# Performance work log

Measured on AMD Instinct MI355X. Metric: run time of the kernel, lower is better.

The kernel has to match this reference:

```python
import jax, jax.numpy as jnp
import numpy as np

G, N = 1024, 40            # graphs, nodes per graph (complete graphs)
SLOPE = 0.1                # leaky relu negative slope
SMAT_IDX = jnp.array([0, 1, 2, 3, 1, 4, 5, 6, 2, 5, 7, 8, 3, 6, 8, 9])


def setup_inputs() -> dict:
    key = jax.random.key(0)
    ks = jax.random.split(key, 24)

    # --- graph structure: G identical complete graphs of N nodes ---
    ii, jj = np.meshgrid(np.arange(N), np.arange(N), indexing="ij")
    mask = ii != jj
    src_l, dst_l = ii[mask], jj[mask]              # directed edges per graph
    offs = (np.arange(G) * N)[:, None]
    edge_index = np.stack([(src_l[None] + offs).ravel(),
                           (dst_l[None] + offs).ravel()]).astype(np.int64)
    iu, ju = np.triu_indices(N, 1)
    M = iu.shape[0]                                 # 780 undirected edges
    ud_edges = np.stack([iu, ju], 1).astype(np.int64)
    edge_map = np.zeros((N, N), np.int64)
    edge_map[iu, ju] = np.arange(M)
    edge_map[ju, iu] = np.arange(M)

    def w(k, shape, fan_in):
        return jax.random.normal(k, shape, jnp.float32) / np.sqrt(fan_in)

    inp = {
        "x": jax.random.normal(ks[0], (G * N, 16), jnp.float32),
        "edge_index": jnp.asarray(edge_index),
        "ud_edges": jnp.asarray(ud_edges),
        "edge_map": jnp.asarray(edge_map),
        # GCN stack 6->32->32->64
        "Wg0": w(ks[1], (6, 32), 6),   "bg0": jnp.zeros((32,), jnp.float32),
        "Wg1": w(ks[2], (32, 32), 32), "bg1": jnp.zeros((32,), jnp.float32),
        "Wg2": w(ks[3], (32, 64), 32), "bg2": jnp.zeros((64,), jnp.float32),
        # node MLP 64->64->64->10
        "Wn0": w(ks[4], (64, 64), 64), "bn0": jnp.zeros((64,), jnp.float32),
        "Wn1": w(ks[5], (64, 64), 64), "bn1": jnp.zeros((64,), jnp.float32),
        "Wn2": w(ks[6], (64, 10), 64), "bn2": jnp.zeros((10,), jnp.float32),
        # edge MLP 64->64->64->10
        "We0": w(ks[7], (64, 64), 64), "be0": jnp.zeros((64,), jnp.float32),
        "We1": w(ks[8], (64, 64), 64), "be1": jnp.zeros((64,), jnp.float32),
        "We2": w(ks[9], (64, 10), 64), "be2": jnp.zeros((10,), jnp.float32),
    }
    return inp


def _forward(x, edge_index, ud_edges, edge_map,
             Wg0, bg0, Wg1, bg1, Wg2, bg2,
             Wn0, bn0, Wn1, bn1, Wn2, bn2,
             We0, be0, We1, be1, We2, be2):
    num_nodes = x.shape[0]
    h = x[:, :6]                                   # node_feature_mode == 1
    src, dst = edge_index[0], edge_index[1]

    # GCN normalization (add_self_loops=False, edge_weight=1)
    deg = jax.ops.segment_sum(jnp.ones(src.shape[0], x.dtype), dst,
                              num_segments=num_nodes)
    dis = jnp.where(deg > 0, jax.lax.rsqrt(jnp.maximum(deg, 1e-12)), 0.0)
    norm = dis[src] * dis[dst]                     # [E]

    def gcn(h, W, b):
        m = (h @ W)[src] * norm[:, None]
        return jax.ops.segment_sum(m, dst, num_segments=num_nodes) + b

    # eval mode: dropout is identity
    h = jax.nn.leaky_relu(gcn(h, Wg0, bg0), SLOPE)
    h = jax.nn.leaky_relu(gcn(h, Wg1, bg1), SLOPE)
    h = gcn(h, Wg2, bg2)                           # [G*N, 64]

    hg = h.reshape(G, N, -1)                       # [G, N, 64]

    def mlp(z, Ws, bs):
        for W, b in zip(Ws[:-1], bs[:-1]):
            z = jax.nn.leaky_relu(z @ W + b, SLOPE)
        return z @ Ws[-1] + bs[-1]

    vp = mlp(hg, [Wn0, Wn1, Wn2], [bn0, bn1, bn2])            # [G, N, 10]
    e = hg[:, ud_edges[:, 0], :] + hg[:, ud_edges[:, 1], :]   # [G, M, 64]
    ep = mlp(e, [We0, We1, We2], [be0, be1, be2])             # [G, M, 10]

    # recover_X: diag blocks smat(vp[i]), off-diag smat(ep[edge_map[i,j]])
    epm = ep[:, edge_map, :]                                  # [G, N, N, 10]
    eye = jnp.eye(N, dtype=bool)[None, :, :, None]
    vecs = jnp.where(eye, vp[:, :, None, :], epm)             # [G, N, N, 10]
    blocks = vecs[..., SMAT_IDX].reshape(G, N, N, 4, 4)
    X = blocks.transpose(0, 1, 3, 2, 4).reshape(G, 4 * N, 4 * N)
    return h, X


def reference(x, edge_index, ud_edges, edge_map,
              Wg0, bg0, Wg1, bg1, Wg2, bg2,
              Wn0, bn0, Wn1, bn1, Wn2, bn2,
              We0, be0, We1, be1, We2, be2):
    return _forward(x, edge_index, ud_edges, edge_map,
                    Wg0, bg0, Wg1, bg1, Wg2, bg2,
                    Wn0, bn0, Wn1, bn1, Wn2, bn2,
                    We0, be0, We1, be1, We2, be2)
```

## Files before the change

### kernel.cpp

```cpp
#include <hip/hip_runtime.h>

#define G_GRAPHS 1024
#define N_NODES  40
#define M_EDGES  780
#define NUM_NODES (G_GRAPHS * N_NODES)
#define H_ELEMS  (NUM_NODES * 64)
#define X_STRIDE 160
#define X_PER_G  25600
#define SLOPE 0.1f

#define EDGE_BLOCKS 6240
#define VP_BLOCKS   320
#define PACK_PER_MLP 9216

typedef __bf16 bf16x8 __attribute__((ext_vector_type(8)));
typedef unsigned short us8 __attribute__((ext_vector_type(8)));
typedef float f32x4 __attribute__((ext_vector_type(4)));

__device__ __forceinline__ float lrelu(float v) { return fmaxf(v, SLOPE * v); }
__device__ __forceinline__ unsigned short f2bf(float x) {
    __bf16 b = (__bf16)x;
    return __builtin_bit_cast(unsigned short, b);
}
__device__ __forceinline__ unsigned int pk2bf(float a, float b) {
    return (unsigned int)f2bf(a) | ((unsigned int)f2bf(b) << 16);
}

__global__ __launch_bounds__(256) void k_prep(const float* __restrict__ We0,
                                              const float* __restrict__ We1,
                                              const float* __restrict__ We2,
                                              const float* __restrict__ Wn0,
                                              const float* __restrict__ Wn1,
                                              const float* __restrict__ Wn2,
                                              unsigned short* __restrict__ wp) {
    int t = blockIdx.x * 256 + threadIdx.x;
    int mlp = t / PACK_PER_MLP;
    int o = t - mlp * PACK_PER_MLP;
    const float* W0 = mlp ? Wn0 : We0;
    const float* W1 = mlp ? Wn1 : We1;
    const float* W2 = mlp ? Wn2 : We2;
    float val;
    if (o < 8192) {
        const float* W = (o < 4096) ? W0 : W1;
        int idx = o & 4095;
        int j = idx & 7, l = (idx >> 3) & 63, tt = idx >> 9;
        int kt = tt & 1, mt = tt >> 1;
        int k = kt * 32 + ((l >> 4) & 3) * 8 + j;
        int m = mt * 16 + (l & 15);
        val = W[k * 64 + m];
    } else {
        int idx = o - 8192;
        int j = idx & 7, l = (idx >> 3) & 63, kt = idx >> 9;
        int k = kt * 32 + ((l >> 4) & 3) * 8 + j;
        int m = l & 15;
        val = (m < 10) ? W2[k * 10 + m] : 0.f;
    }
    wp[mlp * PACK_PER_MLP + o] = f2bf(val);
}

__global__ __launch_bounds__(256) void k_gcn(const float* __restrict__ x,
                                             const float* __restrict__ Wg0,
                                             const float* __restrict__ bg0,
                                             const float* __restrict__ Wg1,
                                             const float* __restrict__ bg1,
                                             const float* __restrict__ Wg2,
                                             const float* __restrict__ bg2,
                                             float* __restrict__ hout) {
    __shared__ float h0[N_NODES * 6];
    __shared__ float buf[N_NODES * 64];
    __shared__ float S[64];
    __shared__ float P[8 * 64];
    __shared__ float h1[N_NODES * 32];
    __shared__ float h2[N_NODES * 32];

    const int g = blockIdx.x;
    const int tid = threadIdx.x;
    const float inv39 = 1.0f / 39.0f;

    for (int idx = tid; idx < N_NODES * 6; idx += 256) {
        int n = idx / 6, f = idx - n * 6;
        h0[idx] = x[(g * N_NODES + n) * 16 + f];
    }
    __syncthreads();

    for (int idx = tid; idx < N_NODES * 32; idx += 256) {
        int n = idx >> 5, c = idx & 31;
        float s = 0.f;
#pragma unroll
        for (int f = 0; f < 6; f++) s += h0[n * 6 + f] * Wg0[f * 32 + c];
        buf[n * 32 + c] = s;
    }
    __syncthreads();
    { int c = tid & 31, grp = tid >> 5; float s = 0.f;
#pragma unroll
      for (int n = grp * 5; n < grp * 5 + 5; n++) s += buf[n * 32 + c];
      P[grp * 32 + c] = s; }
    __syncthreads();
    if (tid < 32) { float s = 0.f;
#pragma unroll
      for (int grp = 0; grp < 8; grp++) s += P[grp * 32 + tid];
      S[tid] = s; }
    __syncthreads();
    for (int idx = tid; idx < N_NODES * 32; idx += 256) {
        int n = idx >> 5, c = idx & 31;
        h1[idx] = lrelu((S[c] - buf[n * 32 + c]) * inv39 + bg0[c]);
    }
    __syncthreads();

    for (int idx = tid; idx < N_NODES * 32; idx += 256) {
        int n = idx >> 5, c = idx & 31;
        float s = 0.f;
#pragma unroll
        for (int m = 0; m < 32; m++) s += h1[n * 32 + m] * Wg1[m * 32 + c];
        buf[n * 32 + c] = s;
    }
    __syncthreads();
    { int c = tid & 31, grp = tid >> 5; float s = 0.f;
#pragma unroll
      for (int n = grp * 5; n < grp * 5 + 5; n++) s += buf[n * 32 + c];
      P[grp * 32 + c] = s; }
    __syncthreads();
    if (tid < 32) { float s = 0.f;
#pragma unroll
      for (int grp = 0; grp < 8; grp++) s += P[grp * 32 + tid];
      S[tid] = s; }
    __syncthreads();
    for (int idx = tid; idx < N_NODES * 32; idx += 256) {
        int n = idx >> 5, c = idx & 31;
        h2[idx] = lrelu((S[c] - buf[n * 32 + c]) * inv39 + bg1[c]);
    }
    __syncthreads();

    for (int idx = tid; idx < N_NODES * 64; idx += 256) {
        int n = idx >> 6, c = idx & 63;
        float s = 0.f;
#pragma unroll
        for (int m = 0; m < 32; m++) s += h2[n * 32 + m] * Wg2[m * 64 + c];
        buf[idx] = s;
    }
    __syncthreads();
    { int c = tid & 63, grp = tid >> 6; float s = 0.f;
#pragma unroll
      for (int n = grp * 10; n < grp * 10 + 10; n++) s += buf[n * 64 + c];
      P[grp * 64 + c] = s; }
    __syncthreads();
    if (tid < 64) { float s = 0.f;
#pragma unroll
      for (int grp = 0; grp < 4; grp++) s += P[grp * 64 + tid];
      S[tid] = s; }
    __syncthreads();
    for (int idx = tid; idx < N_NODES * 64; idx += 256) {
        int n = idx >> 6, c = idx & 63;
        hout[(g * N_NODES + n) * 64 + c] = (S[c] - buf[n * 64 + c]) * inv39 + bg2[c];
    }
}

__global__ __launch_bounds__(256) void k_mlp(const float* __restrict__ h,
                                             const unsigned short* __restrict__ wp,
                                             const float* __restrict__ be0,
                                             const float* __restrict__ be1,
                                             const float* __restrict__ be2,
                                             const float* __restrict__ bn0,
                                             const float* __restrict__ bn1,
                                             const float* __restrict__ bn2,
                                             float* __restrict__ X) {
    __shared__ __align__(16) unsigned short sE[128 * 64];
    __shared__ __align__(16) unsigned short sZ[128 * 64];

    const int tid = threadIdx.x;
    const int l = tid & 63;
    const int w = tid >> 6;
    const int bid = blockIdx.x;
    const bool is_edge = (bid < EDGE_BLOCKS);

    const unsigned short* wb = wp + (is_edge ? 0 : PACK_PER_MLP);
    const float* b0 = is_edge ? be0 : bn0;
    const float* b1 = is_edge ? be1 : bn1;
    const float* b2 = is_edge ? be2 : bn2;

    const int r = 32 * w + (l >> 1);
    const int hf = l & 1;
    int g, i = 0, j = 0;
    if (is_edge) {
        int eid = bid * 128 + r;
        g = eid / M_EDGES;
        int m = eid - g * M_EDGES;
        int rem = m;
        while (rem >= (N_NODES - 1) - i) { rem -= (N_NODES - 1) - i; ++i; }
        j = i + 1 + rem;
    } else {
        int nid = (bid - EDGE_BLOCKS) * 128 + r;
        g = nid / N_NODES;
        i = nid - g * N_NODES;
        j = i;
    }

    {
        const float4* pa = (const float4*)(h + (g * N_NODES + i) * 64 + hf * 32);
        const float4* pb = (const float4*)(h + (g * N_NODES + j) * 64 + hf * 32);
        unsigned short tmp[32];
#pragma unroll
        for (int q = 0; q < 8; q++) {
            float4 a = pa[q];
            if (is_edge) {
                float4 b = pb[q];
                a.x += b.x; a.y += b.y; a.z += b.z; a.w += b.w;
            }
            tmp[4 * q + 0] = f2bf(a.x); tmp[4 * q + 1] = f2bf(a.y);
            tmp[4 * q + 2] = f2bf(a.z); tmp[4 * q + 3] = f2bf(a.w);
        }
#pragma unroll
        for (int q = 0; q < 4; q++) {
            int cs = (hf * 4 + q) ^ (r & 7);
            *(us8*)((char*)sE + r * 128 + cs * 16) = *(const us8*)(tmp + 8 * q);
        }
    }

    const int nl = l & 15;
    const int rq = (l >> 4) & 3;

    auto WA = [&](const unsigned short* base, int mt, int kt) -> bf16x8 {
        return __builtin_bit_cast(bf16x8,
            *(const us8*)(base + ((mt * 2 + kt) * 64 + l) * 8));
    };
    auto ZB = [&](const unsigned short* s, int nt, int kt) -> bf16x8 {
        int node = 32 * w + nt * 16 + nl;
        int cs = (kt * 4 + rq) ^ (node & 7);
        return __builtin_bit_cast(bf16x8,
            *(const us8*)((const char*)s + node * 128 + cs * 16));
    };
    auto zstore = [&](unsigned short* s, int mt, int nt, const f32x4& v) {
        int node = 32 * w + nt * 16 + nl;
        int cs = (mt * 2 + (rq >> 1)) ^ (node & 7);
        uint2 u = make_uint2(pk2bf(v[0], v[1]), pk2bf(v[2], v[3]));
        *(uint2*)((char*)s + node * 128 + cs * 16 + (rq & 1) * 8) = u;
    };

    {
        bf16x8 B[2][2];
#pragma unroll
        for (int nt = 0; nt < 2; nt++)
#pragma unroll
            for (int kt = 0; kt < 2; kt++) B[nt][kt] = ZB(sE, nt, kt);
#pragma unroll
        for (int mt = 0; mt < 4; mt++) {
            bf16x8 A0 = WA(wb, mt, 0), A1 = WA(wb, mt, 1);
            float4 bv = *(const float4*)(b0 + mt * 16 + rq * 4);
#pragma unroll
            for (int nt = 0; nt < 2; nt++) {
                f32x4 acc = (f32x4){0.f, 0.f, 0.f, 0.f};
                acc = __builtin_amdgcn_mfma_f32_16x16x32_bf16(A0, B[nt][0], acc, 0, 0, 0);
                acc = __builtin_amdgcn_mfma_f32_16x16x32_bf16(A1, B[nt][1], acc, 0, 0, 0);
                f32x4 z;
                z[0] = lrelu(acc[0] + bv.x); z[1] = lrelu(acc[1] + bv.y);
                z[2] = lrelu(acc[2] + bv.z); z[3] = lrelu(acc[3] + bv.w);
                zstore(sZ, mt, nt, z);
            }
        }
    }

    {
        bf16x8 B[2][2];
#pragma unroll
        for (int nt = 0; nt < 2; nt++)
#pragma unroll
            for (int kt = 0; kt < 2; kt++) B[nt][kt] = ZB(sZ, nt, kt);
        const unsigned short* w1p = wb + 4096;
#pragma unroll
        for (int mt = 0; mt < 4; mt++) {
            bf16x8 A0 = WA(w1p, mt, 0), A1 = WA(w1p, mt, 1);
            float4 bv = *(const float4*)(b1 + mt * 16 + rq * 4);
#pragma unroll
            for (int nt = 0; nt < 2; nt++) {
                f32x4 acc = (f32x4){0.f, 0.f, 0.f, 0.f};
                acc = __builtin_amdgcn_mfma_f32_16x16x32_bf16(A0, B[nt][0], acc, 0, 0, 0);
                acc = __builtin_amdgcn_mfma_f32_16x16x32_bf16(A1, B[nt][1], acc, 0, 0, 0);
                f32x4 z;
                z[0] = lrelu(acc[0] + bv.x); z[1] = lrelu(acc[1] + bv.y);
                z[2] = lrelu(acc[2] + bv.z); z[3] = lrelu(acc[3] + bv.w);
                zstore(sE, mt, nt, z);
            }
        }
    }

    float* sEPf = (float*)sZ + w * 1024;
    {
        bf16x8 B[2][2];
#pragma unroll
        for (int nt = 0; nt < 2; nt++)
#pragma unroll
            for (int kt = 0; kt < 2; kt++) B[nt][kt] = ZB(sE, nt, kt);
        const unsigned short* w2p = wb + 8192;
        bf16x8 A0 = WA(w2p, 0, 0), A1 = WA(w2p, 0, 1);
        float bz[4];
#pragma unroll
        for (int k = 0; k < 4; k++) {
            int f = rq * 4 + k;
            bz[k] = (f < 10) ? b2[f] : 0.f;
        }
#pragma unroll
        for (int nt = 0; nt < 2; nt++) {
            f32x4 acc = (f32x4){0.f, 0.f, 0.f, 0.f};
            acc = __builtin_amdgcn_mfma_f32_16x16x32_bf16(A0, B[nt][0], acc, 0, 0, 0);
            acc = __builtin_amdgcn_mfma_f32_16x16x32_bf16(A1, B[nt][1], acc, 0, 0, 0);
            int nl2 = nt * 16 + nl;
            float4 v = make_float4(acc[0] + bz[0], acc[1] + bz[1],
                                   acc[2] + bz[2], acc[3] + bz[3]);
            *(float4*)(sEPf + nl2 * 20 + rq * 4) = v;
        }
    }

    {
        const float* ep = sEPf + (r & 31) * 20;
        float4 e0 = *(const float4*)(ep + 0);
        float4 e1 = *(const float4*)(ep + 4);
        float4 e2 = *(const float4*)(ep + 8);
        float4 r0 = make_float4(e0.x, e0.y, e0.z, e0.w);
        float4 r1 = make_float4(e0.y, e1.x, e1.y, e1.z);
        float4 r2 = make_float4(e0.z, e1.y, e1.w, e2.x);
        float4 r3 = make_float4(e0.w, e1.z, e2.x, e2.y);
        float* Xg = X + g * X_PER_G;
        if (is_edge) {
            int bi = hf ? j : i, bj = hf ? i : j;
            float* p = Xg + (4 * bi) * X_STRIDE + 4 * bj;
            *(float4*)(p + 0 * X_STRIDE) = r0;
            *(float4*)(p + 1 * X_STRIDE) = r1;
            *(float4*)(p + 2 * X_STRIDE) = r2;
            *(float4*)(p + 3 * X_STRIDE) = r3;
        } else {
            float* p = Xg + (4 * i + hf * 2) * X_STRIDE + 4 * i;
            if (hf == 0) {
                *(float4*)(p + 0 * X_STRIDE) = r0;
                *(float4*)(p + 1 * X_STRIDE) = r1;
            } else {
                *(float4*)(p + 0 * X_STRIDE) = r2;
                *(float4*)(p + 1 * X_STRIDE) = r3;
            }
        }
    }
}

extern "C" void kernel_launch(void* const* d_in, const int* in_sizes, int n_in,
                              void* d_out, int out_size, void* d_ws, size_t ws_size,
                              hipStream_t stream) {
    const float* x   = (const float*)d_in[0];
    const float* Wg0 = (const float*)d_in[4];
    const float* bg0 = (const float*)d_in[5];
    const float* Wg1 = (const float*)d_in[6];
    const float* bg1 = (const float*)d_in[7];
    const float* Wg2 = (const float*)d_in[8];
    const float* bg2 = (const float*)d_in[9];
    const float* Wn0 = (const float*)d_in[10];
    const float* bn0 = (const float*)d_in[11];
    const float* Wn1 = (const float*)d_in[12];
    const float* bn1 = (const float*)d_in[13];
    const float* Wn2 = (const float*)d_in[14];
    const float* bn2 = (const float*)d_in[15];
    const float* We0 = (const float*)d_in[16];
    const float* be0 = (const float*)d_in[17];
    const float* We1 = (const float*)d_in[18];
    const float* be1 = (const float*)d_in[19];
    const float* We2 = (const float*)d_in[20];
    const float* be2 = (const float*)d_in[21];

    float* hout = (float*)d_out;
    float* X    = hout + H_ELEMS;
    unsigned short* wp = (unsigned short*)d_ws;

    k_prep<<<72, 256, 0, stream>>>(We0, We1, We2, Wn0, Wn1, Wn2, wp);
    k_gcn<<<G_GRAPHS, 256, 0, stream>>>(x, Wg0, bg0, Wg1, bg1, Wg2, bg2, hout);
    k_mlp<<<EDGE_BLOCKS + VP_BLOCKS, 256, 0, stream>>>(hout, wp,
                                                       be0, be1, be2,
                                                       bn0, bn1, bn2, X);
}
```

Baseline: 234.5 us.

## Cache GCN weights in registers, use closed-form edge indexing, share one LDS buffer

The GCN kernel now keeps each thread's weight column and bias in registers and reads the node features as float4 from LDS, replacing repeated global weight loads and index arithmetic. In the MLP kernel the loop that turns an edge id into (i, j) is replaced by a sqrt-based closed form with a one-step correction. The two LDS buffers are merged into one, halving shared memory to allow more blocks per CU. Reusing one buffer is safe only if each wave reads just the rows it writes; otherwise it adds a read-before-overwrite hazard, since no barriers were added.

Result: no change. 231.3 us (-1.3%).

```diff
diff --git a/kernel.cpp b/kernel.cpp
--- a/kernel.cpp
+++ b/kernel.cpp
@@ -58,24 +58,37 @@
     wp[mlp * PACK_PER_MLP + o] = f2bf(val);
 }
 
-__global__ __launch_bounds__(256) void k_gcn(const float* __restrict__ x,
-                                             const float* __restrict__ Wg0,
-                                             const float* __restrict__ bg0,
-                                             const float* __restrict__ Wg1,
-                                             const float* __restrict__ bg1,
-                                             const float* __restrict__ Wg2,
-                                             const float* __restrict__ bg2,
-                                             float* __restrict__ hout) {
-    __shared__ float h0[N_NODES * 6];
-    __shared__ float buf[N_NODES * 64];
+__global__ __launch_bounds__(256, 4) void k_gcn(const float* __restrict__ x,
+                                                const float* __restrict__ Wg0,
+                                                const float* __restrict__ bg0,
+                                                const float* __restrict__ Wg1,
+                                                const float* __restrict__ bg1,
+                                                const float* __restrict__ Wg2,
+                                                const float* __restrict__ bg2,
+                                                float* __restrict__ hout) {
+    __shared__ __align__(16) float h0[N_NODES * 6];
+    __shared__ __align__(16) float buf[N_NODES * 64];
     __shared__ float S[64];
     __shared__ float P[8 * 64];
-    __shared__ float h1[N_NODES * 32];
-    __shared__ float h2[N_NODES * 32];
+    __shared__ __align__(16) float h1[N_NODES * 32];
+    __shared__ __align__(16) float h2[N_NODES * 32];
 
     const int g = blockIdx.x;
     const int tid = threadIdx.x;
     const float inv39 = 1.0f / 39.0f;
+    const int c32 = tid & 31;
+    const int c64 = tid & 63;
+
+    float w0c[6], w1c[32], w2c[32];
+#pragma unroll
+    for (int f = 0; f < 6; f++)  w0c[f] = Wg0[f * 32 + c32];
+#pragma unroll
+    for (int m = 0; m < 32; m++) w1c[m] = Wg1[m * 32 + c32];
+#pragma unroll
+    for (int m = 0; m < 32; m++) w2c[m] = Wg2[m * 64 + c64];
+    const float b0c = bg0[c32];
+    const float b1c = bg1[c32];
+    const float b2c = bg2[c64];
 
     for (int idx = tid; idx < N_NODES * 6; idx += 256) {
         int n = idx / 6, f = idx - n * 6;
@@ -83,76 +96,92 @@
     }
     __syncthreads();
 
-    for (int idx = tid; idx < N_NODES * 32; idx += 256) {
-        int n = idx >> 5, c = idx & 31;
-        float s = 0.f;
-#pragma unroll
-        for (int f = 0; f < 6; f++) s += h0[n * 6 + f] * Wg0[f * 32 + c];
-        buf[n * 32 + c] = s;
-    }
-    __syncthreads();
-    { int c = tid & 31, grp = tid >> 5; float s = 0.f;
-#pragma unroll
-      for (int n = grp * 5; n < grp * 5 + 5; n++) s += buf[n * 32 + c];
-      P[grp * 32 + c] = s; }
+    {
+        int n0 = tid >> 5;
+#pragma unroll
+        for (int t = 0; t < 5; t++) {
+            int n = n0 + 8 * t;
+            float s = 0.f;
+#pragma unroll
+            for (int f = 0; f < 6; f++) s += h0[n * 6 + f] * w0c[f];
+            buf[n * 32 + c32] = s;
+        }
+    }
+    __syncthreads();
+    { int grp = tid >> 5; float s = 0.f;
+#pragma unroll
+      for (int n = grp * 5; n < grp * 5 + 5; n++) s += buf[n * 32 + c32];
+      P[grp * 32 + c32] = s; }
     __syncthreads();
     if (tid < 32) { float s = 0.f;
 #pragma unroll
       for (int grp = 0; grp < 8; grp++) s += P[grp * 32 + tid];
       S[tid] = s; }
     __syncthreads();
-    for (int idx = tid; idx < N_NODES * 32; idx += 256) {
-        int n = idx >> 5, c = idx & 31;
-        h1[idx] = lrelu((S[c] - buf[n * 32 + c]) * inv39 + bg0[c]);
-    }
-    __syncthreads();
-
-    for (int idx = tid; idx < N_NODES * 32; idx += 256) {
-        int n = idx >> 5, c = idx & 31;
-        float s = 0.f;
-#pragma unroll
-        for (int m = 0; m < 32; m++) s += h1[n * 32 + m] * Wg1[m * 32 + c];
-        buf[n * 32 + c] = s;
-    }
-    __syncthreads();
-    { int c = tid & 31, grp = tid >> 5; float s = 0.f;
-#pragma unroll
-      for (int n = grp * 5; n < grp * 5 + 5; n++) s += buf[n * 32 + c];
-      P[grp * 32 + c] = s; }
+    for (int idx = tid; idx < N_NODES * 32; idx += 256)
+        h1[idx] = lrelu((S[c32] - buf[idx]) * inv39 + b0c);
+    __syncthreads();
+
+    {
+        int n0 = tid >> 5;
+#pragma unroll
+        for (int t = 0; t < 5; t++) {
+            int n = n0 + 8 * t;
+            const float4* hp = (const float4*)(h1 + n * 32);
+            float s = 0.f;
+#pragma unroll
+            for (int q = 0; q < 8; q++) {
+                float4 hv = hp[q];
+                s += hv.x * w1c[4 * q + 0] + hv.y * w1c[4 * q + 1]
+                   + hv.z * w1c[4 * q + 2] + hv.w * w1c[4 * q + 3];
+            }
+            buf[n * 32 + c32] = s;
+        }
+    }
+    __syncthreads();
+    { int grp = tid >> 5; float s = 0.f;
+#pragma unroll
+      for (int n = grp * 5; n < grp * 5 + 5; n++) s += buf[n * 32 + c32];
+      P[grp * 32 + c32] = s; }
     __syncthreads();
     if (tid < 32) { float s = 0.f;
 #pragma unroll
       for (int grp = 0; grp < 8; grp++) s += P[grp * 32 + tid];
       S[tid] = s; }
     __syncthreads();
-    for (int idx = tid; idx < N_NODES * 32; idx += 256) {
-        int n = idx >> 5, c = idx & 31;
-        h2[idx] = lrelu((S[c] - buf[n * 32 + c]) * inv39 + bg1[c]);
-    }
-    __syncthreads();
-
-    for (int idx = tid; idx < N_NODES * 64; idx += 256) {
-        int n = idx >> 6, c = idx & 63;
-        float s = 0.f;
-#pragma unroll
-        for (int m = 0; m < 32; m++) s += h2[n * 32 + m] * Wg2[m * 64 + c];
-        buf[idx] = s;
-    }
-    __syncthreads();
-    { int c = tid & 63, grp = tid >> 6; float s = 0.f;
-#pragma unroll
-      for (int n = grp * 10; n < grp * 10 + 10; n++) s += buf[n * 64 + c];
-      P[grp * 64 + c] = s; }
+    for (int idx = tid; idx < N_NODES * 32; idx += 256)
+        h2[idx] = lrelu((S[c32] - buf[idx]) * inv39 + b1c);
+    __syncthreads();
+
+    {
+        int n0 = tid >> 6;
+#pragma unroll
+        for (int t = 0; t < 10; t++) {
+            int n = n0 + 4 * t;
+            const float4* hp = (const float4*)(h2 + n * 32);
+            float s = 0.f;
+#pragma unroll
+            for (int q = 0; q < 8; q++) {
+                float4 hv = hp[q];
+                s += hv.x * w2c[4 * q + 0] + hv.y * w2c[4 * q + 1]
+                   + hv.z * w2c[4 * q + 2] + hv.w * w2c[4 * q + 3];
+            }
+            buf[n * 64 + c64] = s;
+        }
+    }
+    __syncthreads();
+    { int grp = tid >> 6; float s = 0.f;
+#pragma unroll
+      for (int n = grp * 10; n < grp * 10 + 10; n++) s += buf[n * 64 + c64];
+      P[grp * 64 + c64] = s; }
     __syncthreads();
     if (tid < 64) { float s = 0.f;
 #pragma unroll
       for (int grp = 0; grp < 4; grp++) s += P[grp * 64 + tid];
       S[tid] = s; }
     __syncthreads();
-    for (int idx = tid; idx < N_NODES * 64; idx += 256) {
-        int n = idx >> 6, c = idx & 63;
-        hout[(g * N_NODES + n) * 64 + c] = (S[c] - buf[n * 64 + c]) * inv39 + bg2[c];
-    }
+    for (int idx = tid; idx < N_NODES * 64; idx += 256)
+        hout[g * N_NODES * 64 + idx] = (S[c64] - buf[idx]) * inv39 + b2c;
 }
 
 __global__ __launch_bounds__(256) void k_mlp(const float* __restrict__ h,
@@ -164,8 +193,7 @@
                                              const float* __restrict__ bn1,
                                              const float* __restrict__ bn2,
                                              float* __restrict__ X) {
-    __shared__ __align__(16) unsigned short sE[128 * 64];
-    __shared__ __align__(16) unsigned short sZ[128 * 64];
+    __shared__ __align__(16) unsigned short sB[128 * 64];
 
     const int tid = threadIdx.x;
     const int l = tid & 63;
@@ -185,9 +213,14 @@
         int eid = bid * 128 + r;
         g = eid / M_EDGES;
         int m = eid - g * M_EDGES;
-        int rem = m;
-        while (rem >= (N_NODES - 1) - i) { rem -= (N_NODES - 1) - i; ++i; }
-        j = i + 1 + rem;
+        float t = 6241.0f - 8.0f * (float)m;
+        int i0 = (int)(0.5f * (79.0f - sqrtf(t)));
+        i0 = min(38, max(0, i0));
+        int cum = 39 * i0 - ((i0 * (i0 - 1)) >> 1);
+        if (cum > m) { --i0; cum = 39 * i0 - ((i0 * (i0 - 1)) >> 1); }
+        else if (m - cum >= 39 - i0) { cum += 39 - i0; ++i0; }
+        i = i0;
+        j = i0 + 1 + (m - cum);
     } else {
         int nid = (bid - EDGE_BLOCKS) * 128 + r;
         g = nid / N_NODES;
@@ -212,7 +245,7 @@
 #pragma unroll
         for (int q = 0; q < 4; q++) {
             int cs = (hf * 4 + q) ^ (r & 7);
-            *(us8*)((char*)sE + r * 128 + cs * 16) = *(const us8*)(tmp + 8 * q);
+            *(us8*)((char*)sB + r * 128 + cs * 16) = *(const us8*)(tmp + 8 * q);
         }
     }
 
@@ -241,7 +274,7 @@
 #pragma unroll
         for (int nt = 0; nt < 2; nt++)
 #pragma unroll
-            for (int kt = 0; kt < 2; kt++) B[nt][kt] = ZB(sE, nt, kt);
+            for (int kt = 0; kt < 2; kt++) B[nt][kt] = ZB(sB, nt, kt);
 #pragma unroll
         for (int mt = 0; mt < 4; mt++) {
             bf16x8 A0 = WA(wb, mt, 0), A1 = WA(wb, mt, 1);
@@ -254,7 +287,7 @@
                 f32x4 z;
                 z[0] = lrelu(acc[0] + bv.x); z[1] = lrelu(acc[1] + bv.y);
                 z[2] = lrelu(acc[2] + bv.z); z[3] = lrelu(acc[3] + bv.w);
-                zstore(sZ, mt, nt, z);
+                zstore(sB, mt, nt, z);
             }
         }
     }
@@ -264,7 +297,7 @@
 #pragma unroll
         for (int nt = 0; nt < 2; nt++)
 #pragma unroll
-            for (int kt = 0; kt < 2; kt++) B[nt][kt] = ZB(sZ, nt, kt);
+            for (int kt = 0; kt < 2; kt++) B[nt][kt] = ZB(sB, nt, kt);
         const unsigned short* w1p = wb + 4096;
 #pragma unroll
         for (int mt = 0; mt < 4; mt++) {
@@ -278,18 +311,18 @@
                 f32x4 z;
                 z[0] = lrelu(acc[0] + bv.x); z[1] = lrelu(acc[1] + bv.y);
                 z[2] = lrelu(acc[2] + bv.z); z[3] = lrelu(acc[3] + bv.w);
-                zstore(sE, mt, nt, z);
-            }
-        }
-    }
-
-    float* sEPf = (float*)sZ + w * 1024;
+                zstore(sB, mt, nt, z);
+            }
+        }
+    }
+
+    float* sEPf = (float*)sB + w * 1024;
     {
         bf16x8 B[2][2];
 #pragma unroll
         for (int nt = 0; nt < 2; nt++)
 #pragma unroll
-            for (int kt = 0; kt < 2; kt++) B[nt][kt] = ZB(sE, nt, kt);
+            for (int kt = 0; kt < 2; kt++) B[nt][kt] = ZB(sB, nt, kt);
         const unsigned short* w2p = wb + 8192;
         bf16x8 A0 = WA(w2p, 0, 0), A1 = WA(w2p, 0, 1);
         float bz[4];
```
